# Optimization experiments

Hardware: AMD Instinct MI355X
Metric: run time of the kernel (lower is better)

The kernel has to match this reference:

```python
import jax, jax.numpy as jnp
import numpy as np

HIDDEN_DIM = 32
EDGE_DIM = 16
EDGE_HIDDEN = 64
N_EDGES = 250000


def setup_inputs() -> dict:
    key = jax.random.key(0)
    k1, k2, k3, k4, k5 = jax.random.split(key, 5)
    h_v = jax.random.normal(k1, (N_EDGES, HIDDEN_DIM), dtype=jnp.float32)
    h_w = jax.random.normal(k2, (N_EDGES, HIDDEN_DIM), dtype=jnp.float32)
    edge_features = jax.random.normal(k3, (N_EDGES, EDGE_DIM), dtype=jnp.float32)
    # Edge-network MLP params: edge_dim -> edge_hidden -> hidden_dim^2
    W1 = jax.random.normal(k4, (EDGE_DIM, EDGE_HIDDEN), dtype=jnp.float32) * (1.0 / np.sqrt(EDGE_DIM))
    b1 = jnp.zeros((EDGE_HIDDEN,), dtype=jnp.float32)
    W2 = jax.random.normal(k5, (EDGE_HIDDEN, HIDDEN_DIM * HIDDEN_DIM), dtype=jnp.float32) * (1.0 / np.sqrt(EDGE_HIDDEN))
    b2 = jnp.zeros((HIDDEN_DIM * HIDDEN_DIM,), dtype=jnp.float32)
    return {"h_v": h_v, "h_w": h_w, "edge_features": edge_features,
            "W1": W1, "b1": b1, "W2": W2, "b2": b2}


def reference(h_v, h_w, edge_features, W1, b1, W2, b2):
    # 1. Edge MLP: (n_edges, edge_dim) -> (n_edges, d*d)
    hdn = jax.nn.relu(edge_features @ W1 + b1)          # (E, edge_hidden)
    A = (hdn @ W2 + b2)                                  # (E, d*d)
    # 2. Reshape to per-edge matrices (E, d, d)
    d = h_w.shape[-1]
    A = A.reshape(-1, d, d)
    # 3. Per-edge matrix-vector product: M = A(e_vw) @ h_w
    messages = jnp.einsum('eij,ej->ei', A, h_w)          # (E, d)
    return messages
```

## Files before the change

### kernel.cpp

```cpp
#include <hip/hip_runtime.h>

typedef unsigned short u16;
typedef _Float16 f16x2 __attribute__((ext_vector_type(2)));
typedef _Float16 f16x8 __attribute__((ext_vector_type(8)));
typedef float    f32x4  __attribute__((ext_vector_type(4)));
typedef float    f32x16 __attribute__((ext_vector_type(16)));


union U4 { uint4 u; f16x8 h; u16 s[8]; };
union HU { f16x2 h2[4]; f16x8 h8; };

__global__ void prep_kernel(const float* __restrict__ W1,
                            const float* __restrict__ W2,
                            const float* __restrict__ b2,
                            u16* __restrict__ ws)
{
    int id = blockIdx.x * 256 + threadIdx.x;
    if (id < 8320) {
        int k2 = id >> 6, l = id & 63;
        int h = l >> 5, col = l & 31;
        U4 o;
        #pragma unroll
        for (int g = 0; g < 2; ++g) {
            int base4 = k2 * 16 + g * 8 + h * 4;
            f32x4 v;
            if (base4 < 2048) {
                int k1 = base4 >> 5, j32 = base4 & 31;
                v = *(const f32x4*)&W2[k1 * 1024 + col * 32 + j32];
            } else {
                v = *(const f32x4*)&b2[col * 32 + (base4 - 2048)];
            }
            #pragma unroll
            for (int j = 0; j < 4; ++j)
                o.h[g * 4 + j] = (_Float16)v[j];
        }
        *(uint4*)(ws + id * 8) = o.u;
    } else if (id < 8448) {
        int idx = id - 8320;
        int nt = idx >> 6, l = idx & 63;
        int h = l >> 5, col = nt * 32 + (l & 31);
        U4 o;
        #pragma unroll
        for (int g = 0; g < 2; ++g)
            #pragma unroll
            for (int j = 0; j < 4; ++j) {
                int k = g * 8 + h * 4 + j;
                o.h[g * 4 + j] = (_Float16)W1[k * 64 + col];
            }
        *(uint4*)(ws + id * 8) = o.u;
    }
}

#define STRIDE_T 66
#define SLICE_T  4352

__global__ __launch_bounds__(256, 4) void edge_kernel(
    const float* __restrict__ h_w,
    const float* __restrict__ ef,
    const float* __restrict__ b1,
    const u16*  __restrict__ ws,
    float* __restrict__ out,
    int E)
{
    __shared__ alignas(16) u16 ldsT[4 * SLICE_T];
    const int tid  = threadIdx.x;
    const int lane = tid & 63;
    const int wv   = tid >> 6;
    const int l31  = lane & 31;
    const int h    = lane >> 5;
    const int tileBase = (blockIdx.x * 4 + wv) * 64;
    if (tileBase >= E) return;
    u16* myT = ldsT + wv * SLICE_T;

    const uint4* Bf  = (const uint4*)ws;
    const uint4* W1f = (const uint4*)(ws + 8320 * 8);
    const uint4* bp  = Bf + lane;

    U4 pipe[4][2];
    #pragma unroll
    for (int p = 0; p < 4; ++p) {
        pipe[p][0].u = bp[(2 * p) * 64];
        pipe[p][1].u = bp[(2 * p + 1) * 64];
    }

    U4 w0, w1;
    w0.u = W1f[lane];
    w1.u = W1f[64 + lane];
    const float bb0 = b1[l31], bb1 = b1[32 + l31];
    #pragma unroll
    for (int mt = 0; mt < 2; ++mt) {
        int e = tileBase + mt * 32 + l31;
        bool ok = e < E;
        f32x4 g0 = {}, g1 = {};
        if (ok) {
            g0 = *(const f32x4*)&ef[e * 16 + h * 4];
            g1 = *(const f32x4*)&ef[e * 16 + 8 + h * 4];
        }
        U4 a;
        #pragma unroll
        for (int j = 0; j < 4; ++j) {
            a.h[j]     = (_Float16)g0[j];
            a.h[4 + j] = (_Float16)g1[j];
        }
        f32x16 c0 = {}, c1 = {};
        c0 = __builtin_amdgcn_mfma_f32_32x32x16_f16(a.h, w0.h, c0, 0, 0, 0);
        c1 = __builtin_amdgcn_mfma_f32_32x32x16_f16(a.h, w1.h, c1, 0, 0, 0);
        #pragma unroll
        for (int nt = 0; nt < 2; ++nt) {
            float bb = nt ? bb1 : bb0;
            int k1 = nt * 32 + l31;
            #pragma unroll
            for (int rp = 0; rp < 8; ++rp) {
                int r = 2 * rp;
                float v0 = fmaxf((nt ? c1[r]     : c0[r])     + bb, 0.f);
                float v1 = fmaxf((nt ? c1[r + 1] : c0[r + 1]) + bb, 0.f);
                f16x2 p = { (_Float16)v0, (_Float16)v1 };
                int e0 = mt * 32 + (r & 3) + 8 * (r >> 2) + 4 * h;
                *(unsigned int*)(myT + k1 * STRIDE_T + e0) =
                    __builtin_bit_cast(unsigned int, p);
            }
        }
    }
    if (lane < 32)
        *(unsigned int*)(myT + 64 * STRIDE_T + lane * 2) = 0x3C003C00u;

    f16x2 hwA[2][2][4];
    #pragma unroll
    for (int mt = 0; mt < 2; ++mt) {
        int e = tileBase + mt * 32 + l31;
        bool ok = e < E;
        f32x4 q0 = {}, q1 = {}, q2 = {}, q3 = {};
        if (ok) {
            const float* hp = h_w + (size_t)e * 32 + h * 4;
            q0 = *(const f32x4*)(hp);
            q1 = *(const f32x4*)(hp + 8);
            q2 = *(const f32x4*)(hp + 16);
            q3 = *(const f32x4*)(hp + 24);
        }
        hwA[mt][0][0] = f16x2{ (_Float16)q0[0], (_Float16)q0[1] };
        hwA[mt][0][1] = f16x2{ (_Float16)q0[2], (_Float16)q0[3] };
        hwA[mt][0][2] = f16x2{ (_Float16)q1[0], (_Float16)q1[1] };
        hwA[mt][0][3] = f16x2{ (_Float16)q1[2], (_Float16)q1[3] };
        hwA[mt][1][0] = f16x2{ (_Float16)q2[0], (_Float16)q2[1] };
        hwA[mt][1][1] = f16x2{ (_Float16)q2[2], (_Float16)q2[3] };
        hwA[mt][1][2] = f16x2{ (_Float16)q3[0], (_Float16)q3[1] };
        hwA[mt][1][3] = f16x2{ (_Float16)q3[2], (_Float16)q3[3] };
    }

    f32x16 acc0 = {}, acc1 = {};

    u16 t0 = myT[l31];
    u16 t1 = myT[32 + l31];
    #pragma unroll 4
    for (int k1 = 0; k1 < 65; ++k1) {
        const int slot = k1 & 3;
        const u16 c0v = t0, c1v = t1;
        {
            int kn = (k1 + 1 <= 64) ? k1 + 1 : 64;
            t0 = myT[kn * STRIDE_T + l31];
            t1 = myT[kn * STRIDE_T + 32 + l31];
        }
        #pragma unroll
        for (int mt = 0; mt < 2; ++mt) {
            union { u16 u; _Float16 f; } cv;
            cv.u = (mt == 0) ? c0v : c1v;
            f16x2 hh = { cv.f, cv.f };
            HU A;
            #pragma unroll
            for (int rr = 0; rr < 4; ++rr) A.h2[rr] = hh * hwA[mt][0][rr];
            if (mt == 0) acc0 = __builtin_amdgcn_mfma_f32_32x32x16_f16(A.h8, pipe[slot][0].h, acc0, 0, 0, 0);
            else         acc1 = __builtin_amdgcn_mfma_f32_32x32x16_f16(A.h8, pipe[slot][0].h, acc1, 0, 0, 0);
            #pragma unroll
            for (int rr = 0; rr < 4; ++rr) A.h2[rr] = hh * hwA[mt][1][rr];
            if (mt == 0) acc0 = __builtin_amdgcn_mfma_f32_32x32x16_f16(A.h8, pipe[slot][1].h, acc0, 0, 0, 0);
            else         acc1 = __builtin_amdgcn_mfma_f32_32x32x16_f16(A.h8, pipe[slot][1].h, acc1, 0, 0, 0);
        }
        {
            int kp = (k1 + 4 <= 64) ? k1 + 4 : 64;
            pipe[slot][0].u = bp[(2 * kp) * 64];
            pipe[slot][1].u = bp[(2 * kp + 1) * 64];
        }
    }

    #pragma unroll
    for (int mt = 0; mt < 2; ++mt) {
        #pragma unroll
        for (int r = 0; r < 16; ++r) {
            int row = (r & 3) + 8 * (r >> 2) + 4 * h;
            int e = tileBase + mt * 32 + row;
            float v = (mt == 0) ? acc0[r] : acc1[r];
            if (e < E) out[(size_t)e * 32 + l31] = v;
        }
    }
}

extern "C" void kernel_launch(void* const* d_in, const int* in_sizes, int n_in,
                              void* d_out, int out_size, void* d_ws, size_t ws_size,
                              hipStream_t stream)
{
    const float* h_w = (const float*)d_in[1];
    const float* ef  = (const float*)d_in[2];
    const float* W1  = (const float*)d_in[3];
    const float* b1  = (const float*)d_in[4];
    const float* W2  = (const float*)d_in[5];
    const float* b2  = (const float*)d_in[6];
    float* out = (float*)d_out;
    const int E = in_sizes[1] / 32;
    u16* ws = (u16*)d_ws;

    prep_kernel<<<33, 256, 0, stream>>>(W1, W2, b2, ws);

    const int blocks = (E + 4 * 64 - 1) / (4 * 64);
    edge_kernel<<<blocks, 256, 0, stream>>>(h_w, ef, b1, ws, out, E);
}
```

Measured before the change: 47.29 us.

## Stage shared W2 fragments into LDS with double-buffered global_load_lds

Replaces the per-wave register pipeline that reloaded W2/b2 fragments from global memory with block-cooperative async global-to-LDS copies, double-buffered in 8 KB chunks with a __syncthreads per chunk. All four waves now share one copy of the weight stream from LDS instead of each wave fetching it separately. The cost is extra LDS per block, block-wide barriers inside the main loop, and occupancy lowered to 3 blocks per SM in launch bounds. The early exit for out-of-range tiles is removed so every wave reaches the barriers.

```diff
diff --git a/kernel.cpp b/kernel.cpp
--- a/kernel.cpp
+++ b/kernel.cpp
@@ -53,8 +53,25 @@
 
 #define STRIDE_T 66
 #define SLICE_T  4352
-
-__global__ __launch_bounds__(256, 4) void edge_kernel(
+#define B_U16    8192
+
+__device__ __forceinline__ void stage16(const void* g, void* l) {
+    __builtin_amdgcn_global_load_lds(
+        (const __attribute__((address_space(1))) void*)g,
+        (__attribute__((address_space(3))) void*)l, 16, 0, 0);
+}
+
+#define MT_BODY(accv, hh, hwv, B0, B1) do {                                   \
+    HU A_;                                                                    \
+    A_.h2[0] = hh * hwv[0][0]; A_.h2[1] = hh * hwv[0][1];                     \
+    A_.h2[2] = hh * hwv[0][2]; A_.h2[3] = hh * hwv[0][3];                     \
+    accv = __builtin_amdgcn_mfma_f32_32x32x16_f16(A_.h8, B0, accv, 0, 0, 0);  \
+    A_.h2[0] = hh * hwv[1][0]; A_.h2[1] = hh * hwv[1][1];                     \
+    A_.h2[2] = hh * hwv[1][2]; A_.h2[3] = hh * hwv[1][3];                     \
+    accv = __builtin_amdgcn_mfma_f32_32x32x16_f16(A_.h8, B1, accv, 0, 0, 0);  \
+} while (0)
+
+__global__ __launch_bounds__(256, 3) void edge_kernel(
     const float* __restrict__ h_w,
     const float* __restrict__ ef,
     const float* __restrict__ b1,
@@ -62,26 +79,24 @@
     float* __restrict__ out,
     int E)
 {
-    __shared__ alignas(16) u16 ldsT[4 * SLICE_T];
+    __shared__ alignas(16) u16 shm[B_U16 + 4 * SLICE_T];
     const int tid  = threadIdx.x;
     const int lane = tid & 63;
     const int wv   = tid >> 6;
     const int l31  = lane & 31;
     const int h    = lane >> 5;
     const int tileBase = (blockIdx.x * 4 + wv) * 64;
-    if (tileBase >= E) return;
-    u16* myT = ldsT + wv * SLICE_T;
-
-    const uint4* Bf  = (const uint4*)ws;
+    u16* myT = shm + B_U16 + wv * SLICE_T;
+    const char* wsb = (const char*)ws;
+    char*       shb = (char*)shm;
+
+    {
+        int off = wv * 2048;
+        stage16(wsb + off + lane * 16,        shb + off);
+        stage16(wsb + off + 1024 + lane * 16, shb + off + 1024);
+    }
+
     const uint4* W1f = (const uint4*)(ws + 8320 * 8);
-    const uint4* bp  = Bf + lane;
-
-    U4 pipe[4][2];
-    #pragma unroll
-    for (int p = 0; p < 4; ++p) {
-        pipe[p][0].u = bp[(2 * p) * 64];
-        pipe[p][1].u = bp[(2 * p + 1) * 64];
-    }
 
     U4 w0, w1;
     w0.u = W1f[lane];
@@ -149,36 +164,60 @@
 
     f32x16 acc0 = {}, acc1 = {};
 
-    u16 t0 = myT[l31];
-    u16 t1 = myT[32 + l31];
-    #pragma unroll 4
-    for (int k1 = 0; k1 < 65; ++k1) {
-        const int slot = k1 & 3;
-        const u16 c0v = t0, c1v = t1;
-        {
-            int kn = (k1 + 1 <= 64) ? k1 + 1 : 64;
-            t0 = myT[kn * STRIDE_T + l31];
-            t1 = myT[kn * STRIDE_T + 32 + l31];
-        }
-        #pragma unroll
-        for (int mt = 0; mt < 2; ++mt) {
-            union { u16 u; _Float16 f; } cv;
-            cv.u = (mt == 0) ? c0v : c1v;
-            f16x2 hh = { cv.f, cv.f };
-            HU A;
-            #pragma unroll
-            for (int rr = 0; rr < 4; ++rr) A.h2[rr] = hh * hwA[mt][0][rr];
-            if (mt == 0) acc0 = __builtin_amdgcn_mfma_f32_32x32x16_f16(A.h8, pipe[slot][0].h, acc0, 0, 0, 0);
-            else         acc1 = __builtin_amdgcn_mfma_f32_32x32x16_f16(A.h8, pipe[slot][0].h, acc1, 0, 0, 0);
-            #pragma unroll
-            for (int rr = 0; rr < 4; ++rr) A.h2[rr] = hh * hwA[mt][1][rr];
-            if (mt == 0) acc0 = __builtin_amdgcn_mfma_f32_32x32x16_f16(A.h8, pipe[slot][1].h, acc0, 0, 0, 0);
-            else         acc1 = __builtin_amdgcn_mfma_f32_32x32x16_f16(A.h8, pipe[slot][1].h, acc1, 0, 0, 0);
-        }
-        {
-            int kp = (k1 + 4 <= 64) ? k1 + 4 : 64;
-            pipe[slot][0].u = bp[(2 * kp) * 64];
-            pipe[slot][1].u = bp[(2 * kp + 1) * 64];
+    __syncthreads();
+
+    for (int c = 0; c < 16; ++c) {
+        {
+            int cb  = (c + 1 < 16) ? 8192 : 2048;
+            int src = (c + 1) * 8192;
+            int bb  = ((c + 1) & 1) * 8192;
+            #pragma unroll
+            for (int j = 0; j < 2; ++j) {
+                int off = wv * 2048 + j * 1024;
+                if (off < cb)
+                    stage16(wsb + src + off + lane * 16, shb + bb + off);
+            }
+        }
+        {
+            const char* bB = shb + (c & 1) * 8192;
+            #pragma unroll
+            for (int q = 0; q < 4; ++q) {
+                int k1 = c * 4 + q;
+                U4 bf0, bf1;
+                bf0.u = *(const uint4*)(bB + (2 * q) * 1024 + lane * 16);
+                bf1.u = *(const uint4*)(bB + (2 * q + 1) * 1024 + lane * 16);
+                u16 t0v = myT[k1 * STRIDE_T + l31];
+                u16 t1v = myT[k1 * STRIDE_T + 32 + l31];
+                {
+                    _Float16 f0 = __builtin_bit_cast(_Float16, t0v);
+                    f16x2 hh = { f0, f0 };
+                    MT_BODY(acc0, hh, hwA[0], bf0.h, bf1.h);
+                }
+                {
+                    _Float16 f1 = __builtin_bit_cast(_Float16, t1v);
+                    f16x2 hh = { f1, f1 };
+                    MT_BODY(acc1, hh, hwA[1], bf0.h, bf1.h);
+                }
+            }
+        }
+        __syncthreads();
+    }
+    {
+        const char* bB = shb;
+        U4 bf0, bf1;
+        bf0.u = *(const uint4*)(bB + lane * 16);
+        bf1.u = *(const uint4*)(bB + 1024 + lane * 16);
+        u16 t0v = myT[64 * STRIDE_T + l31];
+        u16 t1v = myT[64 * STRIDE_T + 32 + l31];
+        {
+            _Float16 f0 = __builtin_bit_cast(_Float16, t0v);
+            f16x2 hh = { f0, f0 };
+            MT_BODY(acc0, hh, hwA[0], bf0.h, bf1.h);
+        }
+        {
+            _Float16 f1 = __builtin_bit_cast(_Float16, t1v);
+            f16x2 hh = { f1, f1 };
+            MT_BODY(acc1, hh, hwA[1], bf0.h, bf1.h);
         }
     }
 
```

New measurement: 50.40 us. 6.6% more time.

## Stage W2 fragments via double-buffered LDS and keep hidden activations in registers

Applied to the files above, without the earlier changes.

The W2-derived B fragments are now shared by all four waves of a block. They are staged into LDS with global_load_lds in double-buffered chunks under block-wide barriers, replacing the per-wave global register pipeline. The first-layer MFMA is transposed so the ReLU hidden values stay in registers, exchanged between lane halves with a shuffle, instead of going through a per-wave LDS transpose. The b1 bias is pre-permuted by the prep kernel. This cuts redundant global/L2 traffic for the weights and the LDS round trip. In exchange it adds __syncthreads per chunk, raises register pressure (occupancy hint lowered to 3), and removes the early exit for out-of-range waves.

```diff
diff --git a/kernel.cpp b/kernel.cpp
--- a/kernel.cpp
+++ b/kernel.cpp
@@ -11,6 +11,7 @@
 union HU { f16x2 h2[4]; f16x8 h8; };
 
 __global__ void prep_kernel(const float* __restrict__ W1,
+                            const float* __restrict__ b1,
                             const float* __restrict__ W2,
                             const float* __restrict__ b2,
                             u16* __restrict__ ws)
@@ -48,81 +49,39 @@
                 o.h[g * 4 + j] = (_Float16)W1[k * 64 + col];
             }
         *(uint4*)(ws + id * 8) = o.u;
-    }
-}
-
-#define STRIDE_T 66
-#define SLICE_T  4352
-
-__global__ __launch_bounds__(256, 4) void edge_kernel(
+    } else if (id < 8512) {
+        int idx = id - 8448;
+        int hh = idx >> 5, nt = (idx >> 4) & 1, r = idx & 15;
+        int row = (r & 3) + 8 * (r >> 2) + 4 * hh;
+        ((float*)(ws + 67584))[idx] = b1[nt * 32 + row];
+    }
+}
+
+__device__ __forceinline__ void stage16(const void* g, void* l) {
+    __builtin_amdgcn_global_load_lds(
+        (const __attribute__((address_space(1))) void*)g,
+        (__attribute__((address_space(3))) void*)l, 16, 0, 0);
+}
+
+__global__ __launch_bounds__(256, 3) void edge_kernel(
     const float* __restrict__ h_w,
     const float* __restrict__ ef,
-    const float* __restrict__ b1,
     const u16*  __restrict__ ws,
     float* __restrict__ out,
     int E)
 {
-    __shared__ alignas(16) u16 ldsT[4 * SLICE_T];
+    __shared__ alignas(16) u16 shm[16384];
     const int tid  = threadIdx.x;
     const int lane = tid & 63;
-    const int wv   = tid >> 6;
     const int l31  = lane & 31;
     const int h    = lane >> 5;
-    const int tileBase = (blockIdx.x * 4 + wv) * 64;
-    if (tileBase >= E) return;
-    u16* myT = ldsT + wv * SLICE_T;
-
-    const uint4* Bf  = (const uint4*)ws;
-    const uint4* W1f = (const uint4*)(ws + 8320 * 8);
-    const uint4* bp  = Bf + lane;
-
-    U4 pipe[4][2];
-    #pragma unroll
-    for (int p = 0; p < 4; ++p) {
-        pipe[p][0].u = bp[(2 * p) * 64];
-        pipe[p][1].u = bp[(2 * p + 1) * 64];
-    }
-
-    U4 w0, w1;
-    w0.u = W1f[lane];
-    w1.u = W1f[64 + lane];
-    const float bb0 = b1[l31], bb1 = b1[32 + l31];
-    #pragma unroll
-    for (int mt = 0; mt < 2; ++mt) {
-        int e = tileBase + mt * 32 + l31;
-        bool ok = e < E;
-        f32x4 g0 = {}, g1 = {};
-        if (ok) {
-            g0 = *(const f32x4*)&ef[e * 16 + h * 4];
-            g1 = *(const f32x4*)&ef[e * 16 + 8 + h * 4];
-        }
-        U4 a;
-        #pragma unroll
-        for (int j = 0; j < 4; ++j) {
-            a.h[j]     = (_Float16)g0[j];
-            a.h[4 + j] = (_Float16)g1[j];
-        }
-        f32x16 c0 = {}, c1 = {};
-        c0 = __builtin_amdgcn_mfma_f32_32x32x16_f16(a.h, w0.h, c0, 0, 0, 0);
-        c1 = __builtin_amdgcn_mfma_f32_32x32x16_f16(a.h, w1.h, c1, 0, 0, 0);
-        #pragma unroll
-        for (int nt = 0; nt < 2; ++nt) {
-            float bb = nt ? bb1 : bb0;
-            int k1 = nt * 32 + l31;
-            #pragma unroll
-            for (int rp = 0; rp < 8; ++rp) {
-                int r = 2 * rp;
-                float v0 = fmaxf((nt ? c1[r]     : c0[r])     + bb, 0.f);
-                float v1 = fmaxf((nt ? c1[r + 1] : c0[r + 1]) + bb, 0.f);
-                f16x2 p = { (_Float16)v0, (_Float16)v1 };
-                int e0 = mt * 32 + (r & 3) + 8 * (r >> 2) + 4 * h;
-                *(unsigned int*)(myT + k1 * STRIDE_T + e0) =
-                    __builtin_bit_cast(unsigned int, p);
-            }
-        }
-    }
-    if (lane < 32)
-        *(unsigned int*)(myT + 64 * STRIDE_T + lane * 2) = 0x3C003C00u;
+    const int tileBase = (blockIdx.x * 4 + (tid >> 6)) * 64;
+    const char* wsb = (const char*)ws;
+    char*       shb = (char*)shm;
+
+    #pragma unroll
+    for (int j = 0; j < 4; ++j)
+        stage16(wsb + j * 4096 + tid * 16, shb + j * 4096 + tid * 16);
 
     f16x2 hwA[2][2][4];
     #pragma unroll
@@ -147,39 +106,109 @@
         hwA[mt][1][3] = f16x2{ (_Float16)q3[2], (_Float16)q3[3] };
     }
 
+    const uint4* W1f = (const uint4*)(ws + 8320 * 8);
+    U4 w1f0, w1f1;
+    w1f0.u = W1f[lane];
+    w1f1.u = W1f[64 + lane];
+    const float* b1pf = (const float*)(ws + 67584);
+    f32x4 bv[2][4];
+    #pragma unroll
+    for (int nt = 0; nt < 2; ++nt)
+        #pragma unroll
+        for (int qr = 0; qr < 4; ++qr)
+            bv[nt][qr] = *(const f32x4*)(b1pf + h * 32 + nt * 16 + qr * 4);
+
+    f16x2 Q[2][2][8][2];
+    #pragma unroll
+    for (int mt = 0; mt < 2; ++mt) {
+        int e = tileBase + mt * 32 + l31;
+        bool ok = e < E;
+        f32x4 g0 = {}, g1 = {};
+        if (ok) {
+            g0 = *(const f32x4*)&ef[e * 16 + h * 4];
+            g1 = *(const f32x4*)&ef[e * 16 + 8 + h * 4];
+        }
+        U4 a;
+        #pragma unroll
+        for (int j = 0; j < 4; ++j) {
+            a.h[j]     = (_Float16)g0[j];
+            a.h[4 + j] = (_Float16)g1[j];
+        }
+        f32x16 c0 = {}, c1 = {};
+        c0 = __builtin_amdgcn_mfma_f32_32x32x16_f16(w1f0.h, a.h, c0, 0, 0, 0);
+        c1 = __builtin_amdgcn_mfma_f32_32x32x16_f16(w1f1.h, a.h, c1, 0, 0, 0);
+        #pragma unroll
+        for (int nt = 0; nt < 2; ++nt) {
+            #pragma unroll
+            for (int p = 0; p < 8; ++p) {
+                float r0 = (nt ? c1[2 * p]     : c0[2 * p]);
+                float r1 = (nt ? c1[2 * p + 1] : c0[2 * p + 1]);
+                float v0 = fmaxf(r0 + bv[nt][p >> 1][(2 * p) & 3],     0.f);
+                float v1 = fmaxf(r1 + bv[nt][p >> 1][(2 * p + 1) & 3], 0.f);
+                f16x2 own = { (_Float16)v0, (_Float16)v1 };
+                unsigned swu = __shfl_xor(__builtin_bit_cast(unsigned, own), 32, 64);
+                f16x2 sw = __builtin_bit_cast(f16x2, swu);
+                Q[mt][nt][p][0] = h ? sw : own;
+                Q[mt][nt][p][1] = h ? own : sw;
+            }
+        }
+    }
+
     f32x16 acc0 = {}, acc1 = {};
-
-    u16 t0 = myT[l31];
-    u16 t1 = myT[32 + l31];
-    #pragma unroll 4
-    for (int k1 = 0; k1 < 65; ++k1) {
-        const int slot = k1 & 3;
-        const u16 c0v = t0, c1v = t1;
-        {
-            int kn = (k1 + 1 <= 64) ? k1 + 1 : 64;
-            t0 = myT[kn * STRIDE_T + l31];
-            t1 = myT[kn * STRIDE_T + 32 + l31];
-        }
-        #pragma unroll
-        for (int mt = 0; mt < 2; ++mt) {
-            union { u16 u; _Float16 f; } cv;
-            cv.u = (mt == 0) ? c0v : c1v;
-            f16x2 hh = { cv.f, cv.f };
-            HU A;
-            #pragma unroll
-            for (int rr = 0; rr < 4; ++rr) A.h2[rr] = hh * hwA[mt][0][rr];
-            if (mt == 0) acc0 = __builtin_amdgcn_mfma_f32_32x32x16_f16(A.h8, pipe[slot][0].h, acc0, 0, 0, 0);
-            else         acc1 = __builtin_amdgcn_mfma_f32_32x32x16_f16(A.h8, pipe[slot][0].h, acc1, 0, 0, 0);
-            #pragma unroll
-            for (int rr = 0; rr < 4; ++rr) A.h2[rr] = hh * hwA[mt][1][rr];
-            if (mt == 0) acc0 = __builtin_amdgcn_mfma_f32_32x32x16_f16(A.h8, pipe[slot][1].h, acc0, 0, 0, 0);
-            else         acc1 = __builtin_amdgcn_mfma_f32_32x32x16_f16(A.h8, pipe[slot][1].h, acc1, 0, 0, 0);
-        }
-        {
-            int kp = (k1 + 4 <= 64) ? k1 + 4 : 64;
-            pipe[slot][0].u = bp[(2 * kp) * 64];
-            pipe[slot][1].u = bp[(2 * kp + 1) * 64];
-        }
+    __syncthreads();
+
+    #pragma unroll
+    for (int c = 0; c < 8; ++c) {
+        if (c < 7) {
+            #pragma unroll
+            for (int j = 0; j < 4; ++j)
+                stage16(wsb + (c + 1) * 16384 + j * 4096 + tid * 16,
+                        shb + ((c + 1) & 1) * 16384 + j * 4096 + tid * 16);
+        } else {
+            if (tid < 128)
+                stage16(wsb + 131072 + tid * 16, shb + tid * 16);
+        }
+        const char* bB = shb + (c & 1) * 16384;
+        #pragma unroll
+        for (int qq = 0; qq < 8; ++qq) {
+            const int k1   = c * 8 + qq;
+            const int nt   = k1 >> 5;
+            const int q    = k1 & 31;
+            const int pa   = ((q & 3) >> 1) + 2 * (q >> 3);
+            const int half = q & 1;
+            const int hq   = (q >> 2) & 1;
+            U4 bf0, bf1;
+            bf0.u = *(const uint4*)(bB + (2 * qq) * 1024 + lane * 16);
+            bf1.u = *(const uint4*)(bB + (2 * qq + 1) * 1024 + lane * 16);
+            _Float16 x0 = Q[0][nt][pa][hq][half];
+            _Float16 x1 = Q[1][nt][pa][hq][half];
+            f16x2 hh0 = { x0, x0 }, hh1 = { x1, x1 };
+            HU A0, A1;
+            #pragma unroll
+            for (int rr = 0; rr < 4; ++rr) { A0.h2[rr] = hh0 * hwA[0][0][rr]; A1.h2[rr] = hh1 * hwA[1][0][rr]; }
+            acc0 = __builtin_amdgcn_mfma_f32_32x32x16_f16(A0.h8, bf0.h, acc0, 0, 0, 0);
+            acc1 = __builtin_amdgcn_mfma_f32_32x32x16_f16(A1.h8, bf0.h, acc1, 0, 0, 0);
+            #pragma unroll
+            for (int rr = 0; rr < 4; ++rr) { A0.h2[rr] = hh0 * hwA[0][1][rr]; A1.h2[rr] = hh1 * hwA[1][1][rr]; }
+            acc0 = __builtin_amdgcn_mfma_f32_32x32x16_f16(A0.h8, bf1.h, acc0, 0, 0, 0);
+            acc1 = __builtin_amdgcn_mfma_f32_32x32x16_f16(A1.h8, bf1.h, acc1, 0, 0, 0);
+        }
+        __syncthreads();
+    }
+
+    {
+        U4 bf0, bf1;
+        bf0.u = *(const uint4*)(shb + lane * 16);
+        bf1.u = *(const uint4*)(shb + 1024 + lane * 16);
+        HU A0, A1;
+        #pragma unroll
+        for (int rr = 0; rr < 4; ++rr) { A0.h2[rr] = hwA[0][0][rr]; A1.h2[rr] = hwA[1][0][rr]; }
+        acc0 = __builtin_amdgcn_mfma_f32_32x32x16_f16(A0.h8, bf0.h, acc0, 0, 0, 0);
+        acc1 = __builtin_amdgcn_mfma_f32_32x32x16_f16(A1.h8, bf0.h, acc1, 0, 0, 0);
+        #pragma unroll
+        for (int rr = 0; rr < 4; ++rr) { A0.h2[rr] = hwA[0][1][rr]; A1.h2[rr] = hwA[1][1][rr]; }
+        acc0 = __builtin_amdgcn_mfma_f32_32x32x16_f16(A0.h8, bf1.h, acc0, 0, 0, 0);
+        acc1 = __builtin_amdgcn_mfma_f32_32x32x16_f16(A1.h8, bf1.h, acc1, 0, 0, 0);
     }
 
     #pragma unroll
@@ -208,8 +237,8 @@
     const int E = in_sizes[1] / 32;
     u16* ws = (u16*)d_ws;
 
-    prep_kernel<<<33, 256, 0, stream>>>(W1, W2, b2, ws);
-
-    const int blocks = (E + 4 * 64 - 1) / (4 * 64);
-    edge_kernel<<<blocks, 256, 0, stream>>>(h_w, ef, b1, ws, out, E);
-}
+    prep_kernel<<<34, 256, 0, stream>>>(W1, b1, W2, b2, ws);
+
+    const int blocks = (E + 255) / 256;
+    edge_kernel<<<blocks, 256, 0, stream>>>(h_w, ef, ws, out, E);
+}
```

Measured after the change: 47.25 us. Within noise of the previous version (-0.1%).
